# Optimization experiments

Measured on AMD Instinct MI355X. Metric: run time of the kernel, lower is better.

Reference implementation:

```python
import jax, jax.numpy as jnp
import numpy as np

N, C, H, W = 32, 128, 64, 64
D_BOT, K = 512, 7
EPS = 1e-5


def setup_inputs() -> dict:
    key = jax.random.key(0)
    ks = jax.random.split(key, 4)
    init = lambda k, shape, fan: (jax.random.normal(k, shape, jnp.float32) / np.sqrt(fan).astype(np.float32))
    return {
        "x": jax.random.normal(ks[0], (N, C, H, W), jnp.float32),
        "dw_w": init(ks[1], (C, 1, K, K), K * K),          # depthwise kernel, OIHW with I=1
        "dw_b": jnp.zeros((C,), jnp.float32),
        "gamma": jnp.ones((C,), jnp.float32),
        "beta": jnp.zeros((C,), jnp.float32),
        "pw1_w": init(ks[2], (D_BOT, C), C),               # 1x1 conv == channel matmul
        "pw1_b": jnp.zeros((D_BOT,), jnp.float32),
        "pw2_w": init(ks[3], (C, D_BOT), D_BOT),
        "pw2_b": jnp.zeros((C,), jnp.float32),
    }


def reference(x, dw_w, dw_b, gamma, beta, pw1_w, pw1_b, pw2_w, pw2_b):
    # depthwise 7x7 conv, stride 1, 'same' padding (NCHW)
    y = jax.lax.conv_general_dilated(
        x, dw_w, window_strides=(1, 1), padding="SAME",
        dimension_numbers=("NCHW", "OIHW", "NCHW"),
        feature_group_count=x.shape[1],
    ) + dw_b[None, :, None, None]
    # NCHW -> NHWC for channel LayerNorm
    y = jnp.transpose(y, (0, 2, 3, 1))
    mu = jnp.mean(y, axis=-1, keepdims=True)
    var = jnp.mean(jnp.square(y - mu), axis=-1, keepdims=True)
    y = (y - mu) * jax.lax.rsqrt(var + EPS) * gamma + beta
    # pointwise MLP: 1x1 convs are channel-mixing matmuls
    h = jax.nn.relu(jnp.einsum("nhwc,dc->nhwd", y, pw1_w) + pw1_b)
    o = jnp.einsum("nhwd,cd->nhwc", h, pw2_w) + pw2_b
    # back to NCHW + residual
    return x + jnp.transpose(o, (0, 3, 1, 2))
```

## Files before the change

### kernel.cpp

```cpp
#include <hip/hip_runtime.h>
#include <hip/hip_bf16.h>

#define NB   32
#define CCH  128
#define HH   64
#define WW   64
#define DBOT 512
#define EPS_LN 1e-5f

typedef __attribute__((ext_vector_type(8))) short bf16x8;
typedef __attribute__((ext_vector_type(4))) float f32x4;

__device__ __forceinline__ float bf2f(unsigned short u) {
    return __uint_as_float(((unsigned)u) << 16);
}
__device__ __forceinline__ unsigned short f2bf(float f) {
    __hip_bfloat16 h = __float2bfloat16(f);
    return *(unsigned short*)&h;
}

__global__ __launch_bounds__(256) void wcvt_kernel(
    const float* __restrict__ w1, const float* __restrict__ w2,
    __hip_bfloat16* __restrict__ o1, __hip_bfloat16* __restrict__ o2)
{
    int i = blockIdx.x * 256 + threadIdx.x;
    o1[i] = __float2bfloat16(w1[i]);
    o2[i] = __float2bfloat16(w2[i]);
}

#define XS 76

__global__ __launch_bounds__(256) void dwconv_kernel(
    const float* __restrict__ x, const float* __restrict__ dw_w,
    const float* __restrict__ dw_b, unsigned short* __restrict__ cout)
{
    __shared__ float xs[64 * XS];

    const int t = threadIdx.x;
    const int n = blockIdx.x >> 7;
    const int c = blockIdx.x & 127;

    const float* xp = x + ((size_t)(n * CCH + c) << 12);

    #pragma unroll
    for (int i = 0; i < 4; ++i) {
        int idx = i * 256 + t;
        int r   = idx >> 4;
        int c4  = idx & 15;
        float4 v = ((const float4*)xp)[idx];
        *(float4*)&xs[r * XS + 4 + c4 * 4] = v;
    }
    #pragma unroll
    for (int i = 0; i < 3; ++i) {
        int idx = i * 256 + t;
        int r   = idx / 12;
        int p   = idx % 12;
        int col = (p < 4) ? p : (p + 64);
        xs[r * XS + col] = 0.0f;
    }

    float wgt[49];
    const float* wp = dw_w + c * 49;
    #pragma unroll
    for (int j = 0; j < 49; ++j) wgt[j] = wp[j];
    const float bias = dw_b[c];

    __syncthreads();

    const int h  = t >> 2;
    const int w0 = (t & 3) << 4;

    float acc[16];
    #pragma unroll
    for (int j = 0; j < 16; ++j) acc[j] = bias;

    #pragma unroll
    for (int kh = 0; kh < 7; ++kh) {
        int hh = h + kh - 3;
        if (hh < 0 || hh >= HH) continue;
        float r[24];
        const float* row = &xs[hh * XS + w0];
        #pragma unroll
        for (int j = 0; j < 6; ++j) *(float4*)&r[j * 4] = *(const float4*)&row[j * 4];
        #pragma unroll
        for (int kw = 0; kw < 7; ++kw)
            #pragma unroll
            for (int j = 0; j < 16; ++j)
                acc[j] = fmaf(r[j + kw + 1], wgt[kh * 7 + kw], acc[j]);
    }

    uint4 s0, s1;
    {
        __hip_bfloat162 p0 = __float22bfloat162_rn(make_float2(acc[0],  acc[1]));
        __hip_bfloat162 p1 = __float22bfloat162_rn(make_float2(acc[2],  acc[3]));
        __hip_bfloat162 p2 = __float22bfloat162_rn(make_float2(acc[4],  acc[5]));
        __hip_bfloat162 p3 = __float22bfloat162_rn(make_float2(acc[6],  acc[7]));
        __hip_bfloat162 p4 = __float22bfloat162_rn(make_float2(acc[8],  acc[9]));
        __hip_bfloat162 p5 = __float22bfloat162_rn(make_float2(acc[10], acc[11]));
        __hip_bfloat162 p6 = __float22bfloat162_rn(make_float2(acc[12], acc[13]));
        __hip_bfloat162 p7 = __float22bfloat162_rn(make_float2(acc[14], acc[15]));
        s0.x = *(unsigned*)&p0; s0.y = *(unsigned*)&p1;
        s0.z = *(unsigned*)&p2; s0.w = *(unsigned*)&p3;
        s1.x = *(unsigned*)&p4; s1.y = *(unsigned*)&p5;
        s1.z = *(unsigned*)&p6; s1.w = *(unsigned*)&p7;
    }
    unsigned short* op = cout + ((size_t)((n * 64 + h) * 128 + c) << 6) + w0;
    *(uint4*)op       = s0;
    *(uint4*)(op + 8) = s1;
}

#define HS 136

__global__ __launch_bounds__(256, 4) void mlp_kernel(
    const unsigned short* __restrict__ conv,
    const float* __restrict__ gamma,
    const float* __restrict__ beta,
    const __hip_bfloat16* __restrict__ w1,
    const float* __restrict__ b1,
    const __hip_bfloat16* __restrict__ w2,
    const float* __restrict__ b2,
    const float* __restrict__ x,
    float* __restrict__ out)
{
    __shared__ union {
        unsigned short xs[CCH * 64];
        unsigned short h[64 * HS];
    } u;
    __shared__ float sPart[2][256];
    __shared__ float sMu[64], sRstd[64];

    const int t    = threadIdx.x;
    const int wave = t >> 6;
    const int lane = t & 63;
    const int q    = lane >> 4;
    const int ln   = lane & 15;
    const int wm   = (wave >> 1) * 32;
    const int wn   = (wave & 1) * 64;

    const int n = blockIdx.x >> 6;
    const int h = blockIdx.x & 63;

    {
        const uint4* src = (const uint4*)(conv + ((size_t)blockIdx.x << 13));
        #pragma unroll
        for (int i = 0; i < 4; ++i) {
            int idx = i * 256 + t;
            uint4 v = src[idx];
            *(uint4*)&u.xs[idx * 8] = v;
        }
    }
    __syncthreads();

    {
        const int wI = t & 63, cg = t >> 6;
        float s = 0.f, s2 = 0.f;
        #pragma unroll
        for (int j = 0; j < 32; ++j) {
            float v = bf2f(u.xs[(cg * 32 + j) * 64 + wI]);
            s += v;
            s2 = fmaf(v, v, s2);
        }
        sPart[0][cg * 64 + wI] = s;
        sPart[1][cg * 64 + wI] = s2;
    }
    __syncthreads();
    if (t < 64) {
        float su = 0.f, sq = 0.f;
        #pragma unroll
        for (int g = 0; g < 4; ++g) { su += sPart[0][g * 64 + t]; sq += sPart[1][g * 64 + t]; }
        float mu  = su * (1.0f / 128.0f);
        float var = sq * (1.0f / 128.0f) - mu * mu;
        sMu[t]   = mu;
        sRstd[t] = 1.0f / sqrtf(var + EPS_LN);
    }
    __syncthreads();

    bf16x8 af[2][4];
    #pragma unroll
    for (int mt = 0; mt < 2; ++mt) {
        const int pos = wm + mt * 16 + ln;
        const float mu = sMu[pos], rs = sRstd[pos];
        #pragma unroll
        for (int kb = 0; kb < 4; ++kb) {
            const int c0 = kb * 32 + q * 8;
            float4 g0  = *(const float4*)(gamma + c0);
            float4 g1  = *(const float4*)(gamma + c0 + 4);
            float4 be0 = *(const float4*)(beta + c0);
            float4 be1 = *(const float4*)(beta + c0 + 4);
            float gv[8] = {g0.x, g0.y, g0.z, g0.w, g1.x, g1.y, g1.z, g1.w};
            float bv[8] = {be0.x, be0.y, be0.z, be0.w, be1.x, be1.y, be1.z, be1.w};
            bf16x8 a;
            #pragma unroll
            for (int j = 0; j < 8; ++j) {
                float v = bf2f(u.xs[(c0 + j) * 64 + pos]);
                float r = (v - mu) * rs * gv[j] + bv[j];
                a[j] = (short)f2bf(r);
            }
            af[mt][kb] = a;
        }
    }

    f32x4 oacc[2][4];
    #pragma unroll
    for (int mt = 0; mt < 2; ++mt)
        #pragma unroll
        for (int ct = 0; ct < 4; ++ct) oacc[mt][ct] = (f32x4){0.f, 0.f, 0.f, 0.f};

    for (int dc = 0; dc < 4; ++dc) {
        const int d0 = dc * 128;

        f32x4 hacc[2][4];
        #pragma unroll
        for (int mt = 0; mt < 2; ++mt)
            #pragma unroll
            for (int dt = 0; dt < 4; ++dt) hacc[mt][dt] = (f32x4){0.f, 0.f, 0.f, 0.f};

        #pragma unroll
        for (int kb = 0; kb < 4; ++kb) {
            bf16x8 bw[4];
            #pragma unroll
            for (int dt = 0; dt < 4; ++dt) {
                int d = d0 + wn + dt * 16 + ln;
                bw[dt] = *(const bf16x8*)(w1 + (size_t)d * 128 + kb * 32 + q * 8);
            }
            #pragma unroll
            for (int mt = 0; mt < 2; ++mt)
                #pragma unroll
                for (int dt = 0; dt < 4; ++dt)
                    hacc[mt][dt] = __builtin_amdgcn_mfma_f32_16x16x32_bf16(
                        af[mt][kb], bw[dt], hacc[mt][dt], 0, 0, 0);
        }

        __syncthreads();

        #pragma unroll
        for (int dt = 0; dt < 4; ++dt) {
            const int dl = wn + dt * 16 + ln;
            const float b1v = b1[d0 + dl];
            #pragma unroll
            for (int mt = 0; mt < 2; ++mt) {
                #pragma unroll
                for (int r = 0; r < 4; ++r) {
                    float v = fmaxf(hacc[mt][dt][r] + b1v, 0.0f);
                    u.h[(wm + mt * 16 + q * 4 + r) * HS + dl] = f2bf(v);
                }
            }
        }
        __syncthreads();

        #pragma unroll
        for (int kb = 0; kb < 4; ++kb) {
            bf16x8 ah[2];
            #pragma unroll
            for (int mt = 0; mt < 2; ++mt)
                ah[mt] = *(const bf16x8*)&u.h[(wm + mt * 16 + ln) * HS + kb * 32 + q * 8];
            bf16x8 bw2[4];
            #pragma unroll
            for (int ct = 0; ct < 4; ++ct) {
                int c = wn + ct * 16 + ln;
                bw2[ct] = *(const bf16x8*)(w2 + (size_t)c * DBOT + d0 + kb * 32 + q * 8);
            }
            #pragma unroll
            for (int mt = 0; mt < 2; ++mt)
                #pragma unroll
                for (int ct = 0; ct < 4; ++ct)
                    oacc[mt][ct] = __builtin_amdgcn_mfma_f32_16x16x32_bf16(
                        ah[mt], bw2[ct], oacc[mt][ct], 0, 0, 0);
        }
    }

    #pragma unroll
    for (int ct = 0; ct < 4; ++ct) {
        const int c = wn + ct * 16 + ln;
        const float b2v = b2[c];
        #pragma unroll
        for (int mt = 0; mt < 2; ++mt) {
            size_t base = ((size_t)(n * CCH + c) << 12) + (h << 6) + wm + mt * 16 + q * 4;
            float4 xr = *(const float4*)(x + base);
            float4 o;
            o.x = oacc[mt][ct][0] + b2v + xr.x;
            o.y = oacc[mt][ct][1] + b2v + xr.y;
            o.z = oacc[mt][ct][2] + b2v + xr.z;
            o.w = oacc[mt][ct][3] + b2v + xr.w;
            *(float4*)(out + base) = o;
        }
    }
}

extern "C" void kernel_launch(void* const* d_in, const int* in_sizes, int n_in,
                              void* d_out, int out_size, void* d_ws, size_t ws_size,
                              hipStream_t stream)
{
    const float* x     = (const float*)d_in[0];
    const float* dw_w  = (const float*)d_in[1];
    const float* dw_b  = (const float*)d_in[2];
    const float* gamma = (const float*)d_in[3];
    const float* beta  = (const float*)d_in[4];
    const float* pw1_w = (const float*)d_in[5];
    const float* pw1_b = (const float*)d_in[6];
    const float* pw2_w = (const float*)d_in[7];
    const float* pw2_b = (const float*)d_in[8];
    float* out = (float*)d_out;

    char* ws = (char*)d_ws;
    unsigned short* convb = (unsigned short*)ws;
    __hip_bfloat16* w1b   = (__hip_bfloat16*)(ws + (size_t)33554432);
    __hip_bfloat16* w2b   = (__hip_bfloat16*)(ws + (size_t)33554432 + 131072);

    wcvt_kernel<<<256, 256, 0, stream>>>(pw1_w, pw2_w, w1b, w2b);
    dwconv_kernel<<<NB * CCH, 256, 0, stream>>>(x, dw_w, dw_b, convb);
    mlp_kernel<<<NB * HH, 256, 0, stream>>>(convb, gamma, beta, w1b, pw1_b, w2b, pw2_b, x, out);
}
```

Baseline: 285.9 us.

## Keep MLP hidden activations in registers via transposed MFMA and lane shuffles

The MLP kernel now gives each wave its own 16 positions and computes the transposed products (weights as the A operand, activations as B). The ReLU'd hidden tile is repacked into the next MFMA's B fragment with cross-lane shuffles instead of going through shared memory. This removes the LDS round trip and two block barriers per d-chunk, at the cost of each wave loading the full w1/w2 weight slices and writing the output as scalar stores. The dwconv kernel also gets an occupancy hint and loads its weights through readfirstlane so they are treated as wave-uniform.

```diff
diff --git a/kernel.cpp b/kernel.cpp
--- a/kernel.cpp
+++ b/kernel.cpp
@@ -10,6 +10,7 @@
 
 typedef __attribute__((ext_vector_type(8))) short bf16x8;
 typedef __attribute__((ext_vector_type(4))) float f32x4;
+typedef __attribute__((ext_vector_type(4))) unsigned int u32x4;
 
 __device__ __forceinline__ float bf2f(unsigned short u) {
     return __uint_as_float(((unsigned)u) << 16);
@@ -18,6 +19,13 @@
     __hip_bfloat16 h = __float2bfloat16(f);
     return *(unsigned short*)&h;
 }
+__device__ __forceinline__ unsigned pack2(float lo, float hi) {
+    __hip_bfloat162 p = __float22bfloat162_rn(make_float2(lo, hi));
+    return *(unsigned*)&p;
+}
+__device__ __forceinline__ float uniform_load(const float* p) {
+    return __uint_as_float(__builtin_amdgcn_readfirstlane(__float_as_uint(*p)));
+}
 
 __global__ __launch_bounds__(256) void wcvt_kernel(
     const float* __restrict__ w1, const float* __restrict__ w2,
@@ -30,7 +38,7 @@
 
 #define XS 76
 
-__global__ __launch_bounds__(256) void dwconv_kernel(
+__global__ __launch_bounds__(256, 6) void dwconv_kernel(
     const float* __restrict__ x, const float* __restrict__ dw_w,
     const float* __restrict__ dw_b, unsigned short* __restrict__ cout)
 {
@@ -62,8 +70,8 @@
     float wgt[49];
     const float* wp = dw_w + c * 49;
     #pragma unroll
-    for (int j = 0; j < 49; ++j) wgt[j] = wp[j];
-    const float bias = dw_b[c];
+    for (int j = 0; j < 49; ++j) wgt[j] = uniform_load(wp + j);
+    const float bias = uniform_load(dw_b + c);
 
     __syncthreads();
 
@@ -91,25 +99,21 @@
 
     uint4 s0, s1;
     {
-        __hip_bfloat162 p0 = __float22bfloat162_rn(make_float2(acc[0],  acc[1]));
-        __hip_bfloat162 p1 = __float22bfloat162_rn(make_float2(acc[2],  acc[3]));
-        __hip_bfloat162 p2 = __float22bfloat162_rn(make_float2(acc[4],  acc[5]));
-        __hip_bfloat162 p3 = __float22bfloat162_rn(make_float2(acc[6],  acc[7]));
-        __hip_bfloat162 p4 = __float22bfloat162_rn(make_float2(acc[8],  acc[9]));
-        __hip_bfloat162 p5 = __float22bfloat162_rn(make_float2(acc[10], acc[11]));
-        __hip_bfloat162 p6 = __float22bfloat162_rn(make_float2(acc[12], acc[13]));
-        __hip_bfloat162 p7 = __float22bfloat162_rn(make_float2(acc[14], acc[15]));
-        s0.x = *(unsigned*)&p0; s0.y = *(unsigned*)&p1;
-        s0.z = *(unsigned*)&p2; s0.w = *(unsigned*)&p3;
-        s1.x = *(unsigned*)&p4; s1.y = *(unsigned*)&p5;
-        s1.z = *(unsigned*)&p6; s1.w = *(unsigned*)&p7;
+        unsigned p0 = pack2(acc[0],  acc[1]);
+        unsigned p1 = pack2(acc[2],  acc[3]);
+        unsigned p2 = pack2(acc[4],  acc[5]);
+        unsigned p3 = pack2(acc[6],  acc[7]);
+        unsigned p4 = pack2(acc[8],  acc[9]);
+        unsigned p5 = pack2(acc[10], acc[11]);
+        unsigned p6 = pack2(acc[12], acc[13]);
+        unsigned p7 = pack2(acc[14], acc[15]);
+        s0.x = p0; s0.y = p1; s0.z = p2; s0.w = p3;
+        s1.x = p4; s1.y = p5; s1.z = p6; s1.w = p7;
     }
     unsigned short* op = cout + ((size_t)((n * 64 + h) * 128 + c) << 6) + w0;
     *(uint4*)op       = s0;
     *(uint4*)(op + 8) = s1;
 }
-
-#define HS 136
 
 __global__ __launch_bounds__(256, 4) void mlp_kernel(
     const unsigned short* __restrict__ conv,
@@ -122,10 +126,7 @@
     const float* __restrict__ x,
     float* __restrict__ out)
 {
-    __shared__ union {
-        unsigned short xs[CCH * 64];
-        unsigned short h[64 * HS];
-    } u;
+    __shared__ unsigned short xs[CCH * 64];
     __shared__ float sPart[2][256];
     __shared__ float sMu[64], sRstd[64];
 
@@ -134,8 +135,7 @@
     const int lane = t & 63;
     const int q    = lane >> 4;
     const int ln   = lane & 15;
-    const int wm   = (wave >> 1) * 32;
-    const int wn   = (wave & 1) * 64;
+    const int posb = wave << 4;
 
     const int n = blockIdx.x >> 6;
     const int h = blockIdx.x & 63;
@@ -145,8 +145,7 @@
         #pragma unroll
         for (int i = 0; i < 4; ++i) {
             int idx = i * 256 + t;
-            uint4 v = src[idx];
-            *(uint4*)&u.xs[idx * 8] = v;
+            *(uint4*)&xs[idx * 8] = src[idx];
         }
     }
     __syncthreads();
@@ -156,7 +155,7 @@
         float s = 0.f, s2 = 0.f;
         #pragma unroll
         for (int j = 0; j < 32; ++j) {
-            float v = bf2f(u.xs[(cg * 32 + j) * 64 + wI]);
+            float v = bf2f(xs[(cg * 32 + j) * 64 + wI]);
             s += v;
             s2 = fmaf(v, v, s2);
         }
@@ -175,10 +174,9 @@
     }
     __syncthreads();
 
-    bf16x8 af[2][4];
-    #pragma unroll
-    for (int mt = 0; mt < 2; ++mt) {
-        const int pos = wm + mt * 16 + ln;
+    bf16x8 af[4];
+    {
+        const int pos = posb + ln;
         const float mu = sMu[pos], rs = sRstd[pos];
         #pragma unroll
         for (int kb = 0; kb < 4; ++kb) {
@@ -192,97 +190,76 @@
             bf16x8 a;
             #pragma unroll
             for (int j = 0; j < 8; ++j) {
-                float v = bf2f(u.xs[(c0 + j) * 64 + pos]);
-                float r = (v - mu) * rs * gv[j] + bv[j];
-                a[j] = (short)f2bf(r);
+                float v = bf2f(xs[(c0 + j) * 64 + pos]);
+                a[j] = (short)f2bf((v - mu) * rs * gv[j] + bv[j]);
             }
-            af[mt][kb] = a;
-        }
-    }
-
-    f32x4 oacc[2][4];
-    #pragma unroll
-    for (int mt = 0; mt < 2; ++mt)
-        #pragma unroll
-        for (int ct = 0; ct < 4; ++ct) oacc[mt][ct] = (f32x4){0.f, 0.f, 0.f, 0.f};
+            af[kb] = a;
+        }
+    }
+
+    f32x4 oacc[8];
+    #pragma unroll
+    for (int ct = 0; ct < 8; ++ct) oacc[ct] = (f32x4){0.f, 0.f, 0.f, 0.f};
+
+    const int  srcA = ((q & 1) * 32) + ln;
+    const int  srcB = srcA + 16;
+    const bool hiT  = (q >= 2);
 
     for (int dc = 0; dc < 4; ++dc) {
         const int d0 = dc * 128;
-
-        f32x4 hacc[2][4];
-        #pragma unroll
-        for (int mt = 0; mt < 2; ++mt)
-            #pragma unroll
-            for (int dt = 0; dt < 4; ++dt) hacc[mt][dt] = (f32x4){0.f, 0.f, 0.f, 0.f};
-
-        #pragma unroll
-        for (int kb = 0; kb < 4; ++kb) {
-            bf16x8 bw[4];
-            #pragma unroll
-            for (int dt = 0; dt < 4; ++dt) {
-                int d = d0 + wn + dt * 16 + ln;
-                bw[dt] = *(const bf16x8*)(w1 + (size_t)d * 128 + kb * 32 + q * 8);
+        #pragma unroll
+        for (int kb2 = 0; kb2 < 4; ++kb2) {
+            const int db = d0 + kb2 * 32;
+
+            f32x4 h0 = (f32x4){0.f, 0.f, 0.f, 0.f};
+            f32x4 h1 = (f32x4){0.f, 0.f, 0.f, 0.f};
+            const __hip_bfloat16* w1p = w1 + (size_t)(db + ln) * CCH + q * 8;
+            #pragma unroll
+            for (int kb = 0; kb < 4; ++kb) {
+                bf16x8 a0 = *(const bf16x8*)(w1p + kb * 32);
+                bf16x8 a1 = *(const bf16x8*)(w1p + (size_t)16 * CCH + kb * 32);
+                h0 = __builtin_amdgcn_mfma_f32_16x16x32_bf16(a0, af[kb], h0, 0, 0, 0);
+                h1 = __builtin_amdgcn_mfma_f32_16x16x32_bf16(a1, af[kb], h1, 0, 0, 0);
             }
-            #pragma unroll
-            for (int mt = 0; mt < 2; ++mt)
-                #pragma unroll
-                for (int dt = 0; dt < 4; ++dt)
-                    hacc[mt][dt] = __builtin_amdgcn_mfma_f32_16x16x32_bf16(
-                        af[mt][kb], bw[dt], hacc[mt][dt], 0, 0, 0);
-        }
-
-        __syncthreads();
-
-        #pragma unroll
-        for (int dt = 0; dt < 4; ++dt) {
-            const int dl = wn + dt * 16 + ln;
-            const float b1v = b1[d0 + dl];
-            #pragma unroll
-            for (int mt = 0; mt < 2; ++mt) {
-                #pragma unroll
-                for (int r = 0; r < 4; ++r) {
-                    float v = fmaxf(hacc[mt][dt][r] + b1v, 0.0f);
-                    u.h[(wm + mt * 16 + q * 4 + r) * HS + dl] = f2bf(v);
-                }
+
+            float4 ba = *(const float4*)(b1 + db + q * 4);
+            float4 bb = *(const float4*)(b1 + db + 16 + q * 4);
+            unsigned P00 = pack2(fmaxf(h0[0] + ba.x, 0.f), fmaxf(h0[1] + ba.y, 0.f));
+            unsigned P01 = pack2(fmaxf(h0[2] + ba.z, 0.f), fmaxf(h0[3] + ba.w, 0.f));
+            unsigned P10 = pack2(fmaxf(h1[0] + bb.x, 0.f), fmaxf(h1[1] + bb.y, 0.f));
+            unsigned P11 = pack2(fmaxf(h1[2] + bb.z, 0.f), fmaxf(h1[3] + bb.w, 0.f));
+
+            unsigned w0lo = __shfl(P00, srcA), w1lo = __shfl(P01, srcA);
+            unsigned w2lo = __shfl(P00, srcB), w3lo = __shfl(P01, srcB);
+            unsigned w0hi = __shfl(P10, srcA), w1hi = __shfl(P11, srcA);
+            unsigned w2hi = __shfl(P10, srcB), w3hi = __shfl(P11, srcB);
+            u32x4 bwv;
+            bwv.x = hiT ? w0hi : w0lo;
+            bwv.y = hiT ? w1hi : w1lo;
+            bwv.z = hiT ? w2hi : w2lo;
+            bwv.w = hiT ? w3hi : w3lo;
+            bf16x8 bfrag = __builtin_bit_cast(bf16x8, bwv);
+
+            const __hip_bfloat16* w2p = w2 + (size_t)ln * DBOT + db + q * 8;
+            #pragma unroll
+            for (int ct = 0; ct < 8; ++ct) {
+                bf16x8 aw = *(const bf16x8*)(w2p + (size_t)(ct * 16) * DBOT);
+                oacc[ct] = __builtin_amdgcn_mfma_f32_16x16x32_bf16(aw, bfrag, oacc[ct], 0, 0, 0);
             }
         }
-        __syncthreads();
-
-        #pragma unroll
-        for (int kb = 0; kb < 4; ++kb) {
-            bf16x8 ah[2];
-            #pragma unroll
-            for (int mt = 0; mt < 2; ++mt)
-                ah[mt] = *(const bf16x8*)&u.h[(wm + mt * 16 + ln) * HS + kb * 32 + q * 8];
-            bf16x8 bw2[4];
-            #pragma unroll
-            for (int ct = 0; ct < 4; ++ct) {
-                int c = wn + ct * 16 + ln;
-                bw2[ct] = *(const bf16x8*)(w2 + (size_t)c * DBOT + d0 + kb * 32 + q * 8);
-            }
-            #pragma unroll
-            for (int mt = 0; mt < 2; ++mt)
-                #pragma unroll
-                for (int ct = 0; ct < 4; ++ct)
-                    oacc[mt][ct] = __builtin_amdgcn_mfma_f32_16x16x32_bf16(
-                        ah[mt], bw2[ct], oacc[mt][ct], 0, 0, 0);
-        }
-    }
-
-    #pragma unroll
-    for (int ct = 0; ct < 4; ++ct) {
-        const int c = wn + ct * 16 + ln;
-        const float b2v = b2[c];
-        #pragma unroll
-        for (int mt = 0; mt < 2; ++mt) {
-            size_t base = ((size_t)(n * CCH + c) << 12) + (h << 6) + wm + mt * 16 + q * 4;
-            float4 xr = *(const float4*)(x + base);
-            float4 o;
-            o.x = oacc[mt][ct][0] + b2v + xr.x;
-            o.y = oacc[mt][ct][1] + b2v + xr.y;
-            o.z = oacc[mt][ct][2] + b2v + xr.z;
-            o.w = oacc[mt][ct][3] + b2v + xr.w;
-            *(float4*)(out + base) = o;
+    }
+
+    const size_t nbase = ((size_t)(n * CCH)) << 12;
+    const int hw = (h << 6) + posb + ln;
+    #pragma unroll
+    for (int ct = 0; ct < 8; ++ct) {
+        float4 b2v = *(const float4*)(b2 + ct * 16 + q * 4);
+        float bvv[4] = {b2v.x, b2v.y, b2v.z, b2v.w};
+        #pragma unroll
+        for (int rr = 0; rr < 4; ++rr) {
+            int c = ct * 16 + q * 4 + rr;
+            size_t idx = nbase + ((size_t)c << 12) + hw;
+            out[idx] = oacc[ct][rr] + bvv[rr] + x[idx];
         }
     }
 }
```

Result: slower. 398.9 us (+39.5%).

## Make dwconv and MLP kernels persistent over several tiles with prefetched double buffering

Applied to the files above, without the earlier changes.

The depthwise conv kernel now handles four (n,c) planes per block. It double-buffers the input planes in shared memory, loading the next plane into registers while the current one is convolved, and reads the weights with readfirstlane so they are scalar. The MLP kernel handles two rows per block and prefetches the second row's conv tile into LDS with global_load_lds while the first row's matmuls run. This needs separate xs and h buffers where the old code shared them in a union. Together these aim to hide global-load latency and amortise per-block setup, at the cost of fewer blocks, more LDS per block and raw s_waitcnt barriers.

```diff
diff --git a/kernel.cpp b/kernel.cpp
--- a/kernel.cpp
+++ b/kernel.cpp
@@ -18,6 +18,20 @@
     __hip_bfloat16 h = __float2bfloat16(f);
     return *(unsigned short*)&h;
 }
+__device__ __forceinline__ unsigned pack2(float lo, float hi) {
+    __hip_bfloat162 p = __float22bfloat162_rn(make_float2(lo, hi));
+    return *(unsigned*)&p;
+}
+__device__ __forceinline__ float uniform_load(const float* p) {
+    return __uint_as_float(__builtin_amdgcn_readfirstlane(__float_as_uint(*p)));
+}
+
+#define BAR_LGKM() do { \
+    asm volatile("s_waitcnt lgkmcnt(0)" ::: "memory"); \
+    __builtin_amdgcn_s_barrier(); } while (0)
+#define BAR_VM() do { \
+    asm volatile("s_waitcnt vmcnt(0) lgkmcnt(0)" ::: "memory"); \
+    __builtin_amdgcn_s_barrier(); } while (0)
 
 __global__ __launch_bounds__(256) void wcvt_kernel(
     const float* __restrict__ w1, const float* __restrict__ w2,
@@ -30,83 +44,111 @@
 
 #define XS 76
 
-__global__ __launch_bounds__(256) void dwconv_kernel(
+__global__ __launch_bounds__(256, 4) void dwconv_kernel(
     const float* __restrict__ x, const float* __restrict__ dw_w,
     const float* __restrict__ dw_b, unsigned short* __restrict__ cout)
 {
-    __shared__ float xs[64 * XS];
+    __shared__ float xs2[2][64 * XS];
 
     const int t = threadIdx.x;
-    const int n = blockIdx.x >> 7;
-    const int c = blockIdx.x & 127;
-
-    const float* xp = x + ((size_t)(n * CCH + c) << 12);
 
     #pragma unroll
-    for (int i = 0; i < 4; ++i) {
-        int idx = i * 256 + t;
-        int r   = idx >> 4;
-        int c4  = idx & 15;
-        float4 v = ((const float4*)xp)[idx];
-        *(float4*)&xs[r * XS + 4 + c4 * 4] = v;
-    }
-    #pragma unroll
-    for (int i = 0; i < 3; ++i) {
-        int idx = i * 256 + t;
-        int r   = idx / 12;
-        int p   = idx % 12;
-        int col = (p < 4) ? p : (p + 64);
-        xs[r * XS + col] = 0.0f;
-    }
-
-    float wgt[49];
-    const float* wp = dw_w + c * 49;
-    #pragma unroll
-    for (int j = 0; j < 49; ++j) wgt[j] = wp[j];
-    const float bias = dw_b[c];
-
-    __syncthreads();
+    for (int b = 0; b < 2; ++b) {
+        #pragma unroll
+        for (int i = 0; i < 3; ++i) {
+            int idx = i * 256 + t;
+            int r   = idx / 12;
+            int p   = idx % 12;
+            int col = (p < 4) ? p : (p + 64);
+            xs2[b][r * XS + col] = 0.0f;
+        }
+    }
+
+    float4 st[4];
+    {
+        const int pid0 = blockIdx.x * 4;
+        const float* xp = x + ((size_t)pid0 << 12);
+        #pragma unroll
+        for (int i = 0; i < 4; ++i) st[i] = ((const float4*)xp)[i * 256 + t];
+        #pragma unroll
+        for (int i = 0; i < 4; ++i) {
+            int idx = i * 256 + t;
+            int r   = idx >> 4;
+            int c4  = idx & 15;
+            *(float4*)&xs2[0][r * XS + 4 + c4 * 4] = st[i];
+        }
+    }
+    BAR_LGKM();
 
     const int h  = t >> 2;
     const int w0 = (t & 3) << 4;
 
-    float acc[16];
-    #pragma unroll
-    for (int j = 0; j < 16; ++j) acc[j] = bias;
-
-    #pragma unroll
-    for (int kh = 0; kh < 7; ++kh) {
-        int hh = h + kh - 3;
-        if (hh < 0 || hh >= HH) continue;
-        float r[24];
-        const float* row = &xs[hh * XS + w0];
-        #pragma unroll
-        for (int j = 0; j < 6; ++j) *(float4*)&r[j * 4] = *(const float4*)&row[j * 4];
-        #pragma unroll
-        for (int kw = 0; kw < 7; ++kw)
-            #pragma unroll
-            for (int j = 0; j < 16; ++j)
-                acc[j] = fmaf(r[j + kw + 1], wgt[kh * 7 + kw], acc[j]);
-    }
-
-    uint4 s0, s1;
-    {
-        __hip_bfloat162 p0 = __float22bfloat162_rn(make_float2(acc[0],  acc[1]));
-        __hip_bfloat162 p1 = __float22bfloat162_rn(make_float2(acc[2],  acc[3]));
-        __hip_bfloat162 p2 = __float22bfloat162_rn(make_float2(acc[4],  acc[5]));
-        __hip_bfloat162 p3 = __float22bfloat162_rn(make_float2(acc[6],  acc[7]));
-        __hip_bfloat162 p4 = __float22bfloat162_rn(make_float2(acc[8],  acc[9]));
-        __hip_bfloat162 p5 = __float22bfloat162_rn(make_float2(acc[10], acc[11]));
-        __hip_bfloat162 p6 = __float22bfloat162_rn(make_float2(acc[12], acc[13]));
-        __hip_bfloat162 p7 = __float22bfloat162_rn(make_float2(acc[14], acc[15]));
-        s0.x = *(unsigned*)&p0; s0.y = *(unsigned*)&p1;
-        s0.z = *(unsigned*)&p2; s0.w = *(unsigned*)&p3;
-        s1.x = *(unsigned*)&p4; s1.y = *(unsigned*)&p5;
-        s1.z = *(unsigned*)&p6; s1.w = *(unsigned*)&p7;
-    }
-    unsigned short* op = cout + ((size_t)((n * 64 + h) * 128 + c) << 6) + w0;
-    *(uint4*)op       = s0;
-    *(uint4*)(op + 8) = s1;
+    for (int k = 0; k < 4; ++k) {
+        const int pid = blockIdx.x * 4 + k;
+        const int n   = pid >> 7;
+        const int c   = pid & 127;
+        const int cur = k & 1;
+
+        if (k < 3) {
+            const float* xn = x + ((size_t)(pid + 1) << 12);
+            #pragma unroll
+            for (int i = 0; i < 4; ++i) st[i] = ((const float4*)xn)[i * 256 + t];
+        }
+
+        float wgt[49];
+        const float* wp = dw_w + c * 49;
+        #pragma unroll
+        for (int j = 0; j < 49; ++j) wgt[j] = uniform_load(wp + j);
+        const float bias = uniform_load(dw_b + c);
+
+        float acc[16];
+        #pragma unroll
+        for (int j = 0; j < 16; ++j) acc[j] = bias;
+
+        const float* xsb = xs2[cur];
+        #pragma unroll
+        for (int kh = 0; kh < 7; ++kh) {
+            int hh = h + kh - 3;
+            if (hh < 0 || hh >= HH) continue;
+            float r[24];
+            const float* row = &xsb[hh * XS + w0];
+            #pragma unroll
+            for (int j = 0; j < 6; ++j) *(float4*)&r[j * 4] = *(const float4*)&row[j * 4];
+            #pragma unroll
+            for (int kw = 0; kw < 7; ++kw)
+                #pragma unroll
+                for (int j = 0; j < 16; ++j)
+                    acc[j] = fmaf(r[j + kw + 1], wgt[kh * 7 + kw], acc[j]);
+        }
+
+        uint4 s0, s1;
+        {
+            unsigned p0 = pack2(acc[0],  acc[1]);
+            unsigned p1 = pack2(acc[2],  acc[3]);
+            unsigned p2 = pack2(acc[4],  acc[5]);
+            unsigned p3 = pack2(acc[6],  acc[7]);
+            unsigned p4 = pack2(acc[8],  acc[9]);
+            unsigned p5 = pack2(acc[10], acc[11]);
+            unsigned p6 = pack2(acc[12], acc[13]);
+            unsigned p7 = pack2(acc[14], acc[15]);
+            s0.x = p0; s0.y = p1; s0.z = p2; s0.w = p3;
+            s1.x = p4; s1.y = p5; s1.z = p6; s1.w = p7;
+        }
+        unsigned short* op = cout + ((size_t)((n * 64 + h) * 128 + c) << 6) + w0;
+        *(uint4*)op       = s0;
+        *(uint4*)(op + 8) = s1;
+
+        if (k < 3) {
+            #pragma unroll
+            for (int i = 0; i < 4; ++i) {
+                int idx = i * 256 + t;
+                int r   = idx >> 4;
+                int c4  = idx & 15;
+                *(float4*)&xs2[cur ^ 1][r * XS + 4 + c4 * 4] = st[i];
+            }
+            BAR_LGKM();
+        }
+    }
 }
 
 #define HS 136
@@ -122,10 +164,8 @@
     const float* __restrict__ x,
     float* __restrict__ out)
 {
-    __shared__ union {
-        unsigned short xs[CCH * 64];
-        unsigned short h[64 * HS];
-    } u;
+    __shared__ unsigned short xs[CCH * 64];
+    __shared__ unsigned short hbuf[64 * HS];
     __shared__ float sPart[2][256];
     __shared__ float sMu[64], sRstd[64];
 
@@ -137,153 +177,172 @@
     const int wm   = (wave >> 1) * 32;
     const int wn   = (wave & 1) * 64;
 
-    const int n = blockIdx.x >> 6;
-    const int h = blockIdx.x & 63;
-
     {
-        const uint4* src = (const uint4*)(conv + ((size_t)blockIdx.x << 13));
+        const char* src = (const char*)conv + (((size_t)(blockIdx.x * 2)) << 14);
         #pragma unroll
         for (int i = 0; i < 4; ++i) {
-            int idx = i * 256 + t;
-            uint4 v = src[idx];
-            *(uint4*)&u.xs[idx * 8] = v;
-        }
-    }
-    __syncthreads();
-
-    {
-        const int wI = t & 63, cg = t >> 6;
-        float s = 0.f, s2 = 0.f;
-        #pragma unroll
-        for (int j = 0; j < 32; ++j) {
-            float v = bf2f(u.xs[(cg * 32 + j) * 64 + wI]);
-            s += v;
-            s2 = fmaf(v, v, s2);
-        }
-        sPart[0][cg * 64 + wI] = s;
-        sPart[1][cg * 64 + wI] = s2;
-    }
-    __syncthreads();
-    if (t < 64) {
-        float su = 0.f, sq = 0.f;
-        #pragma unroll
-        for (int g = 0; g < 4; ++g) { su += sPart[0][g * 64 + t]; sq += sPart[1][g * 64 + t]; }
-        float mu  = su * (1.0f / 128.0f);
-        float var = sq * (1.0f / 128.0f) - mu * mu;
-        sMu[t]   = mu;
-        sRstd[t] = 1.0f / sqrtf(var + EPS_LN);
-    }
-    __syncthreads();
-
-    bf16x8 af[2][4];
-    #pragma unroll
-    for (int mt = 0; mt < 2; ++mt) {
-        const int pos = wm + mt * 16 + ln;
-        const float mu = sMu[pos], rs = sRstd[pos];
-        #pragma unroll
-        for (int kb = 0; kb < 4; ++kb) {
-            const int c0 = kb * 32 + q * 8;
-            float4 g0  = *(const float4*)(gamma + c0);
-            float4 g1  = *(const float4*)(gamma + c0 + 4);
-            float4 be0 = *(const float4*)(beta + c0);
-            float4 be1 = *(const float4*)(beta + c0 + 4);
-            float gv[8] = {g0.x, g0.y, g0.z, g0.w, g1.x, g1.y, g1.z, g1.w};
-            float bv[8] = {be0.x, be0.y, be0.z, be0.w, be1.x, be1.y, be1.z, be1.w};
-            bf16x8 a;
-            #pragma unroll
-            for (int j = 0; j < 8; ++j) {
-                float v = bf2f(u.xs[(c0 + j) * 64 + pos]);
-                float r = (v - mu) * rs * gv[j] + bv[j];
-                a[j] = (short)f2bf(r);
-            }
-            af[mt][kb] = a;
-        }
-    }
-
-    f32x4 oacc[2][4];
-    #pragma unroll
-    for (int mt = 0; mt < 2; ++mt)
-        #pragma unroll
-        for (int ct = 0; ct < 4; ++ct) oacc[mt][ct] = (f32x4){0.f, 0.f, 0.f, 0.f};
-
-    for (int dc = 0; dc < 4; ++dc) {
-        const int d0 = dc * 128;
-
-        f32x4 hacc[2][4];
+            int cb = (wave * 4 + i) * 64;
+            __builtin_amdgcn_global_load_lds(
+                (const __attribute__((address_space(1))) void*)(src + (size_t)(cb + lane) * 16),
+                (__attribute__((address_space(3))) void*)(&xs[(wave * 4 + i) * 512]),
+                16, 0, 0);
+        }
+    }
+    BAR_VM();
+
+    for (int k = 0; k < 2; ++k) {
+        const int rid = blockIdx.x * 2 + k;
+        const int n   = rid >> 6;
+        const int h   = rid & 63;
+
+        {
+            const int wI = t & 63, cg = t >> 6;
+            float s = 0.f, s2 = 0.f;
+            #pragma unroll
+            for (int j = 0; j < 32; ++j) {
+                float v = bf2f(xs[(cg * 32 + j) * 64 + wI]);
+                s += v;
+                s2 = fmaf(v, v, s2);
+            }
+            sPart[0][cg * 64 + wI] = s;
+            sPart[1][cg * 64 + wI] = s2;
+        }
+        BAR_LGKM();
+        if (t < 64) {
+            float su = 0.f, sq = 0.f;
+            #pragma unroll
+            for (int g = 0; g < 4; ++g) { su += sPart[0][g * 64 + t]; sq += sPart[1][g * 64 + t]; }
+            float mu  = su * (1.0f / 128.0f);
+            float var = sq * (1.0f / 128.0f) - mu * mu;
+            sMu[t]   = mu;
+            sRstd[t] = 1.0f / sqrtf(var + EPS_LN);
+        }
+        BAR_LGKM();
+
+        bf16x8 af[2][4];
+        #pragma unroll
+        for (int mt = 0; mt < 2; ++mt) {
+            const int pos = wm + mt * 16 + ln;
+            const float mu = sMu[pos], rs = sRstd[pos];
+            #pragma unroll
+            for (int kb = 0; kb < 4; ++kb) {
+                const int c0 = kb * 32 + q * 8;
+                float4 g0  = *(const float4*)(gamma + c0);
+                float4 g1  = *(const float4*)(gamma + c0 + 4);
+                float4 be0 = *(const float4*)(beta + c0);
+                float4 be1 = *(const float4*)(beta + c0 + 4);
+                float gv[8] = {g0.x, g0.y, g0.z, g0.w, g1.x, g1.y, g1.z, g1.w};
+                float bv[8] = {be0.x, be0.y, be0.z, be0.w, be1.x, be1.y, be1.z, be1.w};
+                bf16x8 a;
+                #pragma unroll
+                for (int j = 0; j < 8; ++j) {
+                    float v = bf2f(xs[(c0 + j) * 64 + pos]);
+                    float r = (v - mu) * rs * gv[j] + bv[j];
+                    a[j] = (short)f2bf(r);
+                }
+                af[mt][kb] = a;
+            }
+        }
+
+        f32x4 oacc[2][4];
         #pragma unroll
         for (int mt = 0; mt < 2; ++mt)
             #pragma unroll
-            for (int dt = 0; dt < 4; ++dt) hacc[mt][dt] = (f32x4){0.f, 0.f, 0.f, 0.f};
-
-        #pragma unroll
-        for (int kb = 0; kb < 4; ++kb) {
-            bf16x8 bw[4];
+            for (int ct = 0; ct < 4; ++ct) oacc[mt][ct] = (f32x4){0.f, 0.f, 0.f, 0.f};
+
+        for (int dc = 0; dc < 4; ++dc) {
+            const int d0 = dc * 128;
+
+            f32x4 hacc[2][4];
+            #pragma unroll
+            for (int mt = 0; mt < 2; ++mt)
+                #pragma unroll
+                for (int dt = 0; dt < 4; ++dt) hacc[mt][dt] = (f32x4){0.f, 0.f, 0.f, 0.f};
+
+            #pragma unroll
+            for (int kb = 0; kb < 4; ++kb) {
+                bf16x8 bw[4];
+                #pragma unroll
+                for (int dt = 0; dt < 4; ++dt) {
+                    int d = d0 + wn + dt * 16 + ln;
+                    bw[dt] = *(const bf16x8*)(w1 + (size_t)d * 128 + kb * 32 + q * 8);
+                }
+                #pragma unroll
+                for (int mt = 0; mt < 2; ++mt)
+                    #pragma unroll
+                    for (int dt = 0; dt < 4; ++dt)
+                        hacc[mt][dt] = __builtin_amdgcn_mfma_f32_16x16x32_bf16(
+                            af[mt][kb], bw[dt], hacc[mt][dt], 0, 0, 0);
+            }
+
+            BAR_LGKM();
+
+            if (dc == 0 && k == 0) {
+                const char* src = (const char*)conv + (((size_t)(blockIdx.x * 2 + 1)) << 14);
+                #pragma unroll
+                for (int i = 0; i < 4; ++i) {
+                    int cb = (wave * 4 + i) * 64;
+                    __builtin_amdgcn_global_load_lds(
+                        (const __attribute__((address_space(1))) void*)(src + (size_t)(cb + lane) * 16),
+                        (__attribute__((address_space(3))) void*)(&xs[(wave * 4 + i) * 512]),
+                        16, 0, 0);
+                }
+            }
+
             #pragma unroll
             for (int dt = 0; dt < 4; ++dt) {
-                int d = d0 + wn + dt * 16 + ln;
-                bw[dt] = *(const bf16x8*)(w1 + (size_t)d * 128 + kb * 32 + q * 8);
-            }
-            #pragma unroll
-            for (int mt = 0; mt < 2; ++mt)
-                #pragma unroll
-                for (int dt = 0; dt < 4; ++dt)
-                    hacc[mt][dt] = __builtin_amdgcn_mfma_f32_16x16x32_bf16(
-                        af[mt][kb], bw[dt], hacc[mt][dt], 0, 0, 0);
-        }
-
-        __syncthreads();
-
-        #pragma unroll
-        for (int dt = 0; dt < 4; ++dt) {
-            const int dl = wn + dt * 16 + ln;
-            const float b1v = b1[d0 + dl];
+                const int dl = wn + dt * 16 + ln;
+                const float b1v = b1[d0 + dl];
+                #pragma unroll
+                for (int mt = 0; mt < 2; ++mt) {
+                    #pragma unroll
+                    for (int r = 0; r < 4; ++r) {
+                        float v = fmaxf(hacc[mt][dt][r] + b1v, 0.0f);
+                        hbuf[(wm + mt * 16 + q * 4 + r) * HS + dl] = f2bf(v);
+                    }
+                }
+            }
+            BAR_LGKM();
+
+            #pragma unroll
+            for (int kb = 0; kb < 4; ++kb) {
+                bf16x8 ah[2];
+                #pragma unroll
+                for (int mt = 0; mt < 2; ++mt)
+                    ah[mt] = *(const bf16x8*)&hbuf[(wm + mt * 16 + ln) * HS + kb * 32 + q * 8];
+                bf16x8 bw2[4];
+                #pragma unroll
+                for (int ct = 0; ct < 4; ++ct) {
+                    int c = wn + ct * 16 + ln;
+                    bw2[ct] = *(const bf16x8*)(w2 + (size_t)c * DBOT + d0 + kb * 32 + q * 8);
+                }
+                #pragma unroll
+                for (int mt = 0; mt < 2; ++mt)
+                    #pragma unroll
+                    for (int ct = 0; ct < 4; ++ct)
+                        oacc[mt][ct] = __builtin_amdgcn_mfma_f32_16x16x32_bf16(
+                            ah[mt], bw2[ct], oacc[mt][ct], 0, 0, 0);
+            }
+        }
+
+        #pragma unroll
+        for (int ct = 0; ct < 4; ++ct) {
+            const int c = wn + ct * 16 + ln;
+            const float b2v = b2[c];
             #pragma unroll
             for (int mt = 0; mt < 2; ++mt) {
-                #pragma unroll
-                for (int r = 0; r < 4; ++r) {
-                    float v = fmaxf(hacc[mt][dt][r] + b1v, 0.0f);
-                    u.h[(wm + mt * 16 + q * 4 + r) * HS + dl] = f2bf(v);
-                }
-            }
-        }
-        __syncthreads();
-
-        #pragma unroll
-        for (int kb = 0; kb < 4; ++kb) {
-            bf16x8 ah[2];
-            #pragma unroll
-            for (int mt = 0; mt < 2; ++mt)
-                ah[mt] = *(const bf16x8*)&u.h[(wm + mt * 16 + ln) * HS + kb * 32 + q * 8];
-            bf16x8 bw2[4];
-            #pragma unroll
-            for (int ct = 0; ct < 4; ++ct) {
-                int c = wn + ct * 16 + ln;
-                bw2[ct] = *(const bf16x8*)(w2 + (size_t)c * DBOT + d0 + kb * 32 + q * 8);
-            }
-            #pragma unroll
-            for (int mt = 0; mt < 2; ++mt)
-                #pragma unroll
-                for (int ct = 0; ct < 4; ++ct)
-                    oacc[mt][ct] = __builtin_amdgcn_mfma_f32_16x16x32_bf16(
-                        ah[mt], bw2[ct], oacc[mt][ct], 0, 0, 0);
-        }
-    }
-
-    #pragma unroll
-    for (int ct = 0; ct < 4; ++ct) {
-        const int c = wn + ct * 16 + ln;
-        const float b2v = b2[c];
-        #pragma unroll
-        for (int mt = 0; mt < 2; ++mt) {
-            size_t base = ((size_t)(n * CCH + c) << 12) + (h << 6) + wm + mt * 16 + q * 4;
-            float4 xr = *(const float4*)(x + base);
-            float4 o;
-            o.x = oacc[mt][ct][0] + b2v + xr.x;
-            o.y = oacc[mt][ct][1] + b2v + xr.y;
-            o.z = oacc[mt][ct][2] + b2v + xr.z;
-            o.w = oacc[mt][ct][3] + b2v + xr.w;
-            *(float4*)(out + base) = o;
-        }
+                size_t base = ((size_t)(n * CCH + c) << 12) + (h << 6) + wm + mt * 16 + q * 4;
+                float4 xr = *(const float4*)(x + base);
+                float4 o;
+                o.x = oacc[mt][ct][0] + b2v + xr.x;
+                o.y = oacc[mt][ct][1] + b2v + xr.y;
+                o.z = oacc[mt][ct][2] + b2v + xr.z;
+                o.w = oacc[mt][ct][3] + b2v + xr.w;
+                *(float4*)(out + base) = o;
+            }
+        }
+
+        if (k == 0) BAR_VM();
     }
 }
 
@@ -308,6 +367,6 @@
     __hip_bfloat16* w2b   = (__hip_bfloat16*)(ws + (size_t)33554432 + 131072);
 
     wcvt_kernel<<<256, 256, 0, stream>>>(pw1_w, pw2_w, w1b, w2b);
-    dwconv_kernel<<<NB * CCH, 256, 0, stream>>>(x, dw_w, dw_b, convb);
-    mlp_kernel<<<NB * HH, 256, 0, stream>>>(convb, gamma, beta, w1b, pw1_b, w2b, pw2_b, x, out);
-}
+    dwconv_kernel<<<1024, 256, 0, stream>>>(x, dw_w, dw_b, convb);
+    mlp_kernel<<<1024, 256, 0, stream>>>(convb, gamma, beta, w1b, pw1_b, w2b, pw2_b, x, out);
+}
```

Measured after the change: 318.4 us. 11.4% more time.
